# Performance work log

Hardware: AMD Instinct MI355X
Metric: run time of the kernel (lower is better)

Reference implementation:

```python
import jax, jax.numpy as jnp
import numpy as np

EPS = 1e-5
K = 20


def _knn_idx(p, k):
    # p: (B, N, C) -> indices of k nearest neighbors (B, N, k), self included
    inner = jnp.einsum('bnc,bmc->bnm', p, p)
    sq = jnp.sum(p * p, axis=-1)  # (B, N)
    neg_dist = 2.0 * inner - sq[:, :, None] - sq[:, None, :]
    return jax.lax.top_k(neg_dist, k)[1]


def _edge_feature(x, k):
    # x: (B, N, C) -> (B, N, k, 2C) = [neighbor - center, center]
    C = x.shape[-1]
    src = x if C in (3, 6) else x[..., 6:9]  # faithful to torch code path
    idx = _knn_idx(src, k)                    # (B, N, k)
    nb = jax.vmap(lambda xb, ib: xb[ib])(x, idx)  # (B, N, k, C)
    ctr = jnp.broadcast_to(x[:, :, None, :], nb.shape)
    return jnp.concatenate([nb - ctr, ctr], axis=-1)


def _block(h, W, g, b, m, v):
    # 1x1 conv (channels-last) + eval-mode BatchNorm + LeakyReLU(0.2)
    z = jnp.einsum('...c,oc->...o', h, W)
    z = (z - m) * jax.lax.rsqrt(v + EPS) * g + b
    return jnp.where(z >= 0, z, 0.2 * z)


def setup_inputs() -> dict:
    key = jax.random.key(0)
    B, N, D, F = 8, 2048, 3, 1024
    ks = jax.random.split(key, 16)
    s = 0.1
    x = jax.random.normal(ks[0], (B, N, D), dtype=jnp.float32)
    W1 = jax.random.normal(ks[1], (64, 2 * D), dtype=jnp.float32) * s
    W2 = jax.random.normal(ks[2], (64, 64), dtype=jnp.float32) * s
    W3 = jax.random.normal(ks[3], (64, 128), dtype=jnp.float32) * s
    W4 = jax.random.normal(ks[4], (64, 64), dtype=jnp.float32) * s
    W5 = jax.random.normal(ks[5], (64, 128), dtype=jnp.float32) * s
    W6 = jax.random.normal(ks[6], (F, 192), dtype=jnp.float32) * s
    # BN params for bn1..bn5 stacked along axis 0
    bng = 1.0 + 0.1 * jax.random.normal(ks[7], (5, 64), dtype=jnp.float32)
    bnb = 0.1 * jax.random.normal(ks[8], (5, 64), dtype=jnp.float32)
    bnm = 0.1 * jax.random.normal(ks[9], (5, 64), dtype=jnp.float32)
    bnv = 0.5 + jax.random.uniform(ks[10], (5, 64), dtype=jnp.float32)
    bn6g = 1.0 + 0.1 * jax.random.normal(ks[11], (F,), dtype=jnp.float32)
    bn6b = 0.1 * jax.random.normal(ks[12], (F,), dtype=jnp.float32)
    bn6m = 0.1 * jax.random.normal(ks[13], (F,), dtype=jnp.float32)
    bn6v = 0.5 + jax.random.uniform(ks[14], (F,), dtype=jnp.float32)
    return {"x": x, "W1": W1, "W2": W2, "W3": W3, "W4": W4, "W5": W5,
            "W6": W6, "bng": bng, "bnb": bnb, "bnm": bnm, "bnv": bnv,
            "bn6g": bn6g, "bn6b": bn6b, "bn6m": bn6m, "bn6v": bn6v}


def reference(x, W1, W2, W3, W4, W5, W6, bng, bnb, bnm, bnv,
              bn6g, bn6b, bn6m, bn6v):
    # x: (B, N, 3) channels-last throughout
    e = _edge_feature(x, K)                    # (B, N, K, 6)
    h = _block(e, W1, bng[0], bnb[0], bnm[0], bnv[0])
    h = _block(h, W2, bng[1], bnb[1], bnm[1], bnv[1])
    x1 = jnp.max(h, axis=2)                    # (B, N, 64)

    e = _edge_feature(x1, K)                   # knn on channels 6:9
    h = _block(e, W3, bng[2], bnb[2], bnm[2], bnv[2])
    h = _block(h, W4, bng[3], bnb[3], bnm[3], bnv[3])
    x2 = jnp.max(h, axis=2)                    # (B, N, 64)

    e = _edge_feature(x2, K)
    h = _block(e, W5, bng[4], bnb[4], bnm[4], bnv[4])
    x3 = jnp.max(h, axis=2)                    # (B, N, 64)

    x4 = jnp.concatenate([x1, x2, x3], axis=-1)  # (B, N, 192)
    z = _block(x4, W6, bn6g, bn6b, bn6m, bn6v)   # (B, N, F)
    g = jnp.max(z, axis=1)                       # (B, F)
    feat = g[:, None, :]                         # (B, 1, F)
    return feat, jnp.transpose(x4, (0, 2, 1))    # x4 as (B, 192, N)
```

## Files before the change

### kernel.cpp

```cpp
#include <hip/hip_runtime.h>
#include <hip/hip_bf16.h>
#include <math.h>

#define B_ 8
#define N_ 2048
#define KNN 20
#define CH 64

typedef unsigned int u32;

__device__ __forceinline__ float lrelu(float z) { return z >= 0.0f ? z : 0.2f * z; }

__device__ __forceinline__ u32 enc_f32(float f) {
  u32 u = __float_as_uint(f);
  return (u & 0x80000000u) ? ~u : (u | 0x80000000u);
}
__device__ __forceinline__ float dec_f32(u32 u) {
  u32 bits = (u & 0x80000000u) ? (u ^ 0x80000000u) : ~u;
  return __uint_as_float(bits);
}

__global__ __launch_bounds__(256) void prep_kernel(
    const float* __restrict__ W2, const float* __restrict__ W3, const float* __restrict__ W4,
    const float* __restrict__ W5, const float* __restrict__ W6,
    float* __restrict__ w2tg, float* __restrict__ w3tg, float* __restrict__ w4tg,
    float* __restrict__ w5tg, float* __restrict__ w6t, u32* __restrict__ gkeys) {
  int i = blockIdx.x * 256 + threadIdx.x;
  if (i < 192 * 1024) {
    int d = i >> 10, cc = i & 1023;
    w6t[i] = W6[cc * 192 + d];
  }
  if (i < 4096) {
    int c_ = i >> 6, cc = i & 63;
    w2tg[cc * 64 + c_] = W2[i];
    w4tg[cc * 64 + c_] = W4[i];
  }
  if (i < 8192) {
    int d = i >> 6, c_ = i & 63;
    w3tg[i] = W3[c_ * 128 + d];
    w5tg[i] = W5[c_ * 128 + d];
    gkeys[i] = 0u;
  }
}

#define QPB 32
#define SL 8
#define CSL (N_ / SL)
#define CAP 31

__global__ __launch_bounds__(256) void knn_kernel(const float* __restrict__ p, int ld, int off,
                                                  int* __restrict__ idxout) {
  __shared__ __align__(16) char arena[64640];
  float4* pts = (float4*)arena;
  int* buf = (int*)(arena + 32896);
  double* dls = (double*)arena;
  int* ils = (int*)(arena + 40960);

  const int b = blockIdx.y;
  const float* pb = p + (size_t)b * N_ * ld + off;
  for (int j = threadIdx.x; j < N_; j += 256) {
    pts[j + (j >> 8)] = make_float4(pb[(size_t)j * ld + 0], pb[(size_t)j * ld + 1],
                                    pb[(size_t)j * ld + 2], 0.f);
  }
  __syncthreads();

  const int t = threadIdx.x & 7;
  const int qloc = threadIdx.x >> 3;
  const int q = blockIdx.x * QPB + qloc;
  const float4 qp = pts[q + (q >> 8)];
  const int jb = t * CSL;
  const float4* myp = pts + jb + t;

  float d0 = 1e30f, d1 = 1e30f, d2 = 1e30f;
#pragma unroll 4
  for (int i = 0; i < CSL; ++i) {
    float4 c = myp[i];
    float dx = qp.x - c.x, dy = qp.y - c.y, dz = qp.z - c.z;
    float d = fmaf(dz, dz, fmaf(dy, dy, dx * dx));
    float lo = fminf(d, d0); float hi = fmaxf(d, d0); d0 = lo;
    float m1 = fminf(d1, hi); float c1 = fmaxf(d1, hi); d1 = m1;
    d2 = fminf(d2, c1);
  }
  float thr = d2;
#pragma unroll
  for (int s = 1; s < 8; s <<= 1) thr = fmaxf(thr, __shfl_xor(thr, s));
  thr = thr * 1.0001f + 1e-7f;

  int cnt = 0;
  int* mybuf = buf + threadIdx.x * CAP;
#pragma unroll 4
  for (int i = 0; i < CSL; ++i) {
    float4 c = myp[i];
    float dx = qp.x - c.x, dy = qp.y - c.y, dz = qp.z - c.z;
    float d = fmaf(dz, dz, fmaf(dy, dy, dx * dx));
    if (d <= thr) {
      if (cnt < CAP) mybuf[cnt] = jb + i;
      ++cnt;
    }
  }

  double ld_[KNN]; int li_[KNN];
#pragma unroll
  for (int u = 0; u < KNN; ++u) { ld_[u] = 1e300; li_[u] = 0x7fffffff; }

  const bool ovf = cnt > CAP;
  const int m = ovf ? 0 : cnt;
  for (int e = 0; e < m; ++e) {
    int j = mybuf[e];
    float4 c = pts[j + (j >> 8)];
    double dx = (double)qp.x - (double)c.x;
    double dy = (double)qp.y - (double)c.y;
    double dz = (double)qp.z - (double)c.z;
    double d = dx * dx + dy * dy + dz * dz;
    if (d < ld_[KNN - 1]) {
      ld_[KNN - 1] = d; li_[KNN - 1] = j;
#pragma unroll
      for (int u = KNN - 1; u > 0; --u) {
        if (ld_[u] < ld_[u - 1]) {
          double td = ld_[u]; ld_[u] = ld_[u - 1]; ld_[u - 1] = td;
          int ti = li_[u]; li_[u] = li_[u - 1]; li_[u - 1] = ti;
        }
      }
    }
  }
  if (ovf) {
    for (int i = 0; i < CSL; ++i) {
      int j = jb + i;
      float4 c = myp[i];
      double dx = (double)qp.x - (double)c.x;
      double dy = (double)qp.y - (double)c.y;
      double dz = (double)qp.z - (double)c.z;
      double d = dx * dx + dy * dy + dz * dz;
      if (d < ld_[KNN - 1]) {
        ld_[KNN - 1] = d; li_[KNN - 1] = j;
#pragma unroll
        for (int u = KNN - 1; u > 0; --u) {
          if (ld_[u] < ld_[u - 1]) {
            double td = ld_[u]; ld_[u] = ld_[u - 1]; ld_[u - 1] = td;
            int ti = li_[u]; li_[u] = li_[u - 1]; li_[u - 1] = ti;
          }
        }
      }
    }
  }
  __syncthreads();
#pragma unroll
  for (int u = 0; u < KNN; ++u) {
    dls[threadIdx.x * KNN + u] = ld_[u];
    ils[threadIdx.x * KNN + u] = li_[u];
  }
  __syncthreads();

  if (t == 0) {
    int h0 = 0, h1 = 0, h2 = 0, h3 = 0, h4 = 0, h5 = 0, h6 = 0, h7 = 0;
    const int lb = qloc * 8;
    int* outp = idxout + ((size_t)b * N_ + q) * KNN;
    for (int r = 0; r < KNN; ++r) {
      double bd = 1e301; int bi = 0x7fffffff; int bt = 0;
#define CONSIDER(T, H)                                                     \
      { int li2 = (lb + (T)) * KNN + (H);                                  \
        double dv = dls[li2]; int iv = ils[li2];                           \
        if (dv < bd || (dv == bd && iv < bi)) { bd = dv; bi = iv; bt = (T); } }
      CONSIDER(0, h0) CONSIDER(1, h1) CONSIDER(2, h2) CONSIDER(3, h3)
      CONSIDER(4, h4) CONSIDER(5, h5) CONSIDER(6, h6) CONSIDER(7, h7)
#undef CONSIDER
      outp[r] = bi;
      h0 += (bt == 0); h1 += (bt == 1); h2 += (bt == 2); h3 += (bt == 3);
      h4 += (bt == 4); h5 += (bt == 5); h6 += (bt == 6); h7 += (bt == 7);
    }
  }
}

__global__ __launch_bounds__(256) void stage1_kernel(
    const float* __restrict__ x, const int* __restrict__ idx,
    const float* __restrict__ W1, const float* __restrict__ w2tg,
    const float* __restrict__ g0, const float* __restrict__ b0,
    const float* __restrict__ m0, const float* __restrict__ v0,
    const float* __restrict__ g1, const float* __restrict__ b1,
    const float* __restrict__ m1, const float* __restrict__ v1,
    float* __restrict__ x1out) {
  __shared__ float nbs[4][KNN][3];
  __shared__ float ctrs[4][3];
  __shared__ int sidx[4][KNN];
  const int b = blockIdx.y;
  const int n0 = blockIdx.x * 4;
  const int p = threadIdx.x >> 6, c = threadIdx.x & 63;

  for (int i = threadIdx.x; i < 4 * KNN; i += 256)
    sidx[i / KNN][i % KNN] = idx[((size_t)b * N_ + n0 + i / KNN) * KNN + i % KNN];
  __syncthreads();
  for (int i = threadIdx.x; i < 4 * KNN * 3; i += 256) {
    int pp = i / (KNN * 3), r = i % (KNN * 3), k = r / 3, d = r % 3;
    nbs[pp][k][d] = x[((size_t)b * N_ + sidx[pp][k]) * 3 + d];
  }
  if (threadIdx.x < 12) {
    int pp = threadIdx.x / 3, d = threadIdx.x % 3;
    ctrs[pp][d] = x[((size_t)b * N_ + n0 + pp) * 3 + d];
  }
  __syncthreads();

  float sc0, sh0, sc1, sh1;
  {
    double rs = 1.0 / sqrt((double)v0[c] + 1e-5);
    sc0 = (float)((double)g0[c] * rs); sh0 = b0[c] - m0[c] * sc0;
    rs = 1.0 / sqrt((double)v1[c] + 1e-5);
    sc1 = (float)((double)g1[c] * rs); sh1 = b1[c] - m1[c] * sc1;
  }

  const float cx = ctrs[p][0], cy = ctrs[p][1], cz = ctrs[p][2];
  const float wa0 = W1[c * 6 + 0], wa1 = W1[c * 6 + 1], wa2 = W1[c * 6 + 2];
  const float wb0 = W1[c * 6 + 3], wb1 = W1[c * 6 + 4], wb2 = W1[c * 6 + 5];
  const float cbase = cx * wb0 + cy * wb1 + cz * wb2;

  float h1r[KNN];
#pragma unroll
  for (int k = 0; k < KNN; ++k) {
    float a = (nbs[p][k][0] - cx) * wa0 + (nbs[p][k][1] - cy) * wa1 + (nbs[p][k][2] - cz) * wa2 + cbase;
    h1r[k] = lrelu(a * sc0 + sh0);
  }

  float acc2[KNN];
#pragma unroll
  for (int k = 0; k < KNN; ++k) acc2[k] = 0.f;
  for (int cc = 0; cc < CH; ++cc) {
    float w = w2tg[cc * CH + c];
#pragma unroll
    for (int k = 0; k < KNN; ++k) {
      float hv = __int_as_float(__builtin_amdgcn_readlane(__float_as_int(h1r[k]), cc));
      acc2[k] += hv * w;
    }
  }
  float mx = -INFINITY;
#pragma unroll
  for (int k = 0; k < KNN; ++k) mx = fmaxf(mx, lrelu(acc2[k] * sc1 + sh1));
  x1out[((size_t)b * N_ + n0 + p) * CH + c] = mx;
}

__global__ __launch_bounds__(256) void stage2_kernel(
    const float* __restrict__ xin, const int* __restrict__ idx,
    const float* __restrict__ w3tg, const float* __restrict__ w4tg,
    const float* __restrict__ g0, const float* __restrict__ b0,
    const float* __restrict__ m0, const float* __restrict__ v0,
    const float* __restrict__ g1, const float* __restrict__ b1,
    const float* __restrict__ m1, const float* __restrict__ v1,
    float* __restrict__ xout) {
  __shared__ float nbs[4][KNN][CH];
  __shared__ float ctrs[4][CH];
  __shared__ int sidx[4][KNN];
  const int b = blockIdx.y, n0 = blockIdx.x * 4;
  const int p = threadIdx.x >> 6, c = threadIdx.x & 63;

  for (int i = threadIdx.x; i < 4 * KNN; i += 256)
    sidx[i / KNN][i % KNN] = idx[((size_t)b * N_ + n0 + i / KNN) * KNN + i % KNN];
  __syncthreads();
  for (int i = threadIdx.x; i < 4 * KNN * 16; i += 256) {
    int pp = i / (KNN * 16), r = i % (KNN * 16), k = r >> 4, d4 = (r & 15) * 4;
    const float4 v = *(const float4*)&xin[((size_t)b * N_ + sidx[pp][k]) * CH + d4];
    *(float4*)&nbs[pp][k][d4] = v;
  }
  for (int i = threadIdx.x; i < 4 * 16; i += 256) {
    int pp = i / 16, d4 = (i % 16) * 4;
    *(float4*)&ctrs[pp][d4] = *(const float4*)&xin[((size_t)b * N_ + n0 + pp) * CH + d4];
  }
  __syncthreads();

  float sc0, sh0, sc1, sh1;
  {
    double rs = 1.0 / sqrt((double)v0[c] + 1e-5);
    sc0 = (float)((double)g0[c] * rs); sh0 = b0[c] - m0[c] * sc0;
    rs = 1.0 / sqrt((double)v1[c] + 1e-5);
    sc1 = (float)((double)g1[c] * rs); sh1 = b1[c] - m1[c] * sc1;
  }

  float acc[KNN];
#pragma unroll
  for (int k = 0; k < KNN; ++k) acc[k] = 0.f;
  float base = 0.f;
#pragma unroll 4
  for (int d = 0; d < CH; d += 4) {
    float a0 = w3tg[(d + 0) * 64 + c], a1 = w3tg[(d + 1) * 64 + c];
    float a2 = w3tg[(d + 2) * 64 + c], a3 = w3tg[(d + 3) * 64 + c];
    float q0 = w3tg[(64 + d + 0) * 64 + c], q1 = w3tg[(64 + d + 1) * 64 + c];
    float q2 = w3tg[(64 + d + 2) * 64 + c], q3 = w3tg[(64 + d + 3) * 64 + c];
    const float4 ct = *(const float4*)&ctrs[p][d];
    base += ct.x * (q0 - a0) + ct.y * (q1 - a1) + ct.z * (q2 - a2) + ct.w * (q3 - a3);
#pragma unroll
    for (int k = 0; k < KNN; ++k) {
      const float4 nb = *(const float4*)&nbs[p][k][d];
      acc[k] += nb.x * a0 + nb.y * a1 + nb.z * a2 + nb.w * a3;
    }
  }
  float h1r[KNN];
#pragma unroll
  for (int k = 0; k < KNN; ++k) h1r[k] = lrelu((acc[k] + base) * sc0 + sh0);

  float acc2[KNN];
#pragma unroll
  for (int k = 0; k < KNN; ++k) acc2[k] = 0.f;
  for (int cc = 0; cc < CH; ++cc) {
    float w = w4tg[cc * CH + c];
#pragma unroll
    for (int k = 0; k < KNN; ++k) {
      float hv = __int_as_float(__builtin_amdgcn_readlane(__float_as_int(h1r[k]), cc));
      acc2[k] += hv * w;
    }
  }
  float mx = -INFINITY;
#pragma unroll
  for (int k = 0; k < KNN; ++k) mx = fmaxf(mx, lrelu(acc2[k] * sc1 + sh1));
  xout[((size_t)b * N_ + n0 + p) * CH + c] = mx;
}

__global__ __launch_bounds__(256) void stage3_kernel(
    const float* __restrict__ xin, const int* __restrict__ idx,
    const float* __restrict__ w5tg,
    const float* __restrict__ g0, const float* __restrict__ b0,
    const float* __restrict__ m0, const float* __restrict__ v0,
    float* __restrict__ xout) {
  __shared__ float nbs[4][KNN][CH];
  __shared__ float ctrs[4][CH];
  __shared__ int sidx[4][KNN];
  const int b = blockIdx.y, n0 = blockIdx.x * 4;
  const int p = threadIdx.x >> 6, c = threadIdx.x & 63;

  for (int i = threadIdx.x; i < 4 * KNN; i += 256)
    sidx[i / KNN][i % KNN] = idx[((size_t)b * N_ + n0 + i / KNN) * KNN + i % KNN];
  __syncthreads();
  for (int i = threadIdx.x; i < 4 * KNN * 16; i += 256) {
    int pp = i / (KNN * 16), r = i % (KNN * 16), k = r >> 4, d4 = (r & 15) * 4;
    const float4 v = *(const float4*)&xin[((size_t)b * N_ + sidx[pp][k]) * CH + d4];
    *(float4*)&nbs[pp][k][d4] = v;
  }
  for (int i = threadIdx.x; i < 4 * 16; i += 256) {
    int pp = i / 16, d4 = (i % 16) * 4;
    *(float4*)&ctrs[pp][d4] = *(const float4*)&xin[((size_t)b * N_ + n0 + pp) * CH + d4];
  }
  __syncthreads();

  float sc0, sh0;
  {
    double rs = 1.0 / sqrt((double)v0[c] + 1e-5);
    sc0 = (float)((double)g0[c] * rs); sh0 = b0[c] - m0[c] * sc0;
  }

  float acc[KNN];
#pragma unroll
  for (int k = 0; k < KNN; ++k) acc[k] = 0.f;
  float base = 0.f;
#pragma unroll 4
  for (int d = 0; d < CH; d += 4) {
    float a0 = w5tg[(d + 0) * 64 + c], a1 = w5tg[(d + 1) * 64 + c];
    float a2 = w5tg[(d + 2) * 64 + c], a3 = w5tg[(d + 3) * 64 + c];
    float q0 = w5tg[(64 + d + 0) * 64 + c], q1 = w5tg[(64 + d + 1) * 64 + c];
    float q2 = w5tg[(64 + d + 2) * 64 + c], q3 = w5tg[(64 + d + 3) * 64 + c];
    const float4 ct = *(const float4*)&ctrs[p][d];
    base += ct.x * (q0 - a0) + ct.y * (q1 - a1) + ct.z * (q2 - a2) + ct.w * (q3 - a3);
#pragma unroll
    for (int k = 0; k < KNN; ++k) {
      const float4 nb = *(const float4*)&nbs[p][k][d];
      acc[k] += nb.x * a0 + nb.y * a1 + nb.z * a2 + nb.w * a3;
    }
  }
  float mx = -INFINITY;
#pragma unroll
  for (int k = 0; k < KNN; ++k) mx = fmaxf(mx, lrelu((acc[k] + base) * sc0 + sh0));
  xout[((size_t)b * N_ + n0 + p) * CH + c] = mx;
}

__global__ __launch_bounds__(256) void stage6_kernel(
    const float* __restrict__ x1, const float* __restrict__ x2, const float* __restrict__ x3,
    const float* __restrict__ w6t,
    const float* __restrict__ g6, const float* __restrict__ b6,
    const float* __restrict__ m6, const float* __restrict__ v6,
    u32* __restrict__ gkeys) {
  __shared__ float xsT[192][16];
  const int b = blockIdx.y;
  const int n0 = blockIdx.x * 16;
  for (int i = threadIdx.x; i < 16 * 192; i += 256) {
    int d = i >> 4, pp = i & 15;
    float v;
    if (d < 64)       v = x1[((size_t)b * N_ + n0 + pp) * CH + d];
    else if (d < 128) v = x2[((size_t)b * N_ + n0 + pp) * CH + (d - 64)];
    else              v = x3[((size_t)b * N_ + n0 + pp) * CH + (d - 128)];
    xsT[d][pp] = v;
  }
  __syncthreads();

  const int c0 = threadIdx.x << 2;
  float4 acc[16];
#pragma unroll
  for (int pp = 0; pp < 16; ++pp) acc[pp] = make_float4(0.f, 0.f, 0.f, 0.f);

  for (int d = 0; d < 192; ++d) {
    const float4 w = *(const float4*)&w6t[(size_t)d * 1024 + c0];
#pragma unroll
    for (int q = 0; q < 4; ++q) {
      const float4 xq = *(const float4*)&xsT[d][q * 4];
#define ACC4(J, XV) { float4& A = acc[q * 4 + (J)]; A.x += (XV) * w.x; A.y += (XV) * w.y; A.z += (XV) * w.z; A.w += (XV) * w.w; }
      ACC4(0, xq.x) ACC4(1, xq.y) ACC4(2, xq.z) ACC4(3, xq.w)
#undef ACC4
    }
  }

  const float4 gg = *(const float4*)&g6[c0];
  const float4 bb = *(const float4*)&b6[c0];
  const float4 mm = *(const float4*)&m6[c0];
  const float4 vv = *(const float4*)&v6[c0];
  float4 s, h;
  s.x = (float)((double)gg.x / sqrt((double)vv.x + 1e-5)); h.x = bb.x - mm.x * s.x;
  s.y = (float)((double)gg.y / sqrt((double)vv.y + 1e-5)); h.y = bb.y - mm.y * s.y;
  s.z = (float)((double)gg.z / sqrt((double)vv.z + 1e-5)); h.z = bb.z - mm.z * s.z;
  s.w = (float)((double)gg.w / sqrt((double)vv.w + 1e-5)); h.w = bb.w - mm.w * s.w;

  float4 mx = make_float4(-INFINITY, -INFINITY, -INFINITY, -INFINITY);
#pragma unroll
  for (int pp = 0; pp < 16; ++pp) {
    mx.x = fmaxf(mx.x, lrelu(acc[pp].x * s.x + h.x));
    mx.y = fmaxf(mx.y, lrelu(acc[pp].y * s.y + h.y));
    mx.z = fmaxf(mx.z, lrelu(acc[pp].z * s.z + h.z));
    mx.w = fmaxf(mx.w, lrelu(acc[pp].w * s.w + h.w));
  }
  u32* gk = gkeys + (size_t)b * 1024 + c0;
  atomicMax(&gk[0], enc_f32(mx.x));
  atomicMax(&gk[1], enc_f32(mx.y));
  atomicMax(&gk[2], enc_f32(mx.z));
  atomicMax(&gk[3], enc_f32(mx.w));
}

__global__ __launch_bounds__(256) void feat_kernel(const u32* __restrict__ gkeys, float* __restrict__ out) {
  int i = blockIdx.x * 256 + threadIdx.x;
  if (i < 8192) out[i] = dec_f32(gkeys[i]);
}

__global__ __launch_bounds__(256) void xpose_kernel(
    const float* __restrict__ x1, const float* __restrict__ x2, const float* __restrict__ x3,
    float* __restrict__ out) {
  __shared__ float tile[64][65];
  const int b = blockIdx.y;
  const int n0 = blockIdx.x * 64;
  const float* srcs[3] = {x1, x2, x3};
#pragma unroll
  for (int s = 0; s < 3; ++s) {
    const float* src = srcs[s];
    {
      const int row = threadIdx.x >> 2, cb = (threadIdx.x & 3) * 16;
      const float4* rp = (const float4*)&src[((size_t)b * N_ + n0 + row) * CH + cb];
      float4 v0 = rp[0], v1 = rp[1], v2 = rp[2], v3 = rp[3];
      float* tp = &tile[row][cb];
      tp[0] = v0.x; tp[1] = v0.y; tp[2] = v0.z; tp[3] = v0.w;
      tp[4] = v1.x; tp[5] = v1.y; tp[6] = v1.z; tp[7] = v1.w;
      tp[8] = v2.x; tp[9] = v2.y; tp[10] = v2.z; tp[11] = v2.w;
      tp[12] = v3.x; tp[13] = v3.y; tp[14] = v3.z; tp[15] = v3.w;
    }
    __syncthreads();
    {
      const int n = threadIdx.x & 63;
      const int cg = (threadIdx.x >> 6) * 16;
      for (int c = cg; c < cg + 16; ++c)
        out[((size_t)b * 192 + s * 64 + c) * N_ + n0 + n] = tile[n][c];
    }
    __syncthreads();
  }
}

extern "C" void kernel_launch(void* const* d_in, const int* in_sizes, int n_in,
                              void* d_out, int out_size, void* d_ws, size_t ws_size,
                              hipStream_t stream) {
  const float* x   = (const float*)d_in[0];
  const float* W1  = (const float*)d_in[1];
  const float* W2  = (const float*)d_in[2];
  const float* W3  = (const float*)d_in[3];
  const float* W4  = (const float*)d_in[4];
  const float* W5  = (const float*)d_in[5];
  const float* W6  = (const float*)d_in[6];
  const float* bng = (const float*)d_in[7];
  const float* bnb = (const float*)d_in[8];
  const float* bnm = (const float*)d_in[9];
  const float* bnv = (const float*)d_in[10];
  const float* g6  = (const float*)d_in[11];
  const float* b6  = (const float*)d_in[12];
  const float* m6  = (const float*)d_in[13];
  const float* v6  = (const float*)d_in[14];
  float* out = (float*)d_out;

  float* ws = (float*)d_ws;
  float* x1b  = ws;
  float* x2b  = x1b + 1048576;
  float* x3b  = x2b + 1048576;
  float* w6t  = x3b + 1048576;
  float* w2tg = w6t + 196608;
  float* w4tg = w2tg + 4096;
  float* w3tg = w4tg + 4096;
  float* w5tg = w3tg + 8192;
  u32*   gkeys = (u32*)(w5tg + 8192);
  int*   idxb  = (int*)(gkeys + 8192);

  prep_kernel<<<768, 256, 0, stream>>>(W2, W3, W4, W5, W6, w2tg, w3tg, w4tg, w5tg, w6t, gkeys);

  knn_kernel<<<dim3(N_ / QPB, B_), 256, 0, stream>>>(x, 3, 0, idxb);
  stage1_kernel<<<dim3(N_ / 4, B_), 256, 0, stream>>>(
      x, idxb, W1, w2tg,
      bng + 0, bnb + 0, bnm + 0, bnv + 0,
      bng + 64, bnb + 64, bnm + 64, bnv + 64, x1b);

  knn_kernel<<<dim3(N_ / QPB, B_), 256, 0, stream>>>(x1b, 64, 6, idxb);
  stage2_kernel<<<dim3(N_ / 4, B_), 256, 0, stream>>>(
      x1b, idxb, w3tg, w4tg,
      bng + 128, bnb + 128, bnm + 128, bnv + 128,
      bng + 192, bnb + 192, bnm + 192, bnv + 192, x2b);

  knn_kernel<<<dim3(N_ / QPB, B_), 256, 0, stream>>>(x2b, 64, 6, idxb);
  stage3_kernel<<<dim3(N_ / 4, B_), 256, 0, stream>>>(
      x2b, idxb, w5tg,
      bng + 256, bnb + 256, bnm + 256, bnv + 256, x3b);

  stage6_kernel<<<dim3(N_ / 16, B_), 256, 0, stream>>>(x1b, x2b, x3b, w6t, g6, b6, m6, v6, gkeys);
  feat_kernel<<<32, 256, 0, stream>>>(gkeys, out);
  xpose_kernel<<<dim3(N_ / 64, B_), 256, 0, stream>>>(x1b, x2b, x3b, out + 8192);
}
```

Before: 791.2 us.

## Compute stage3 edge conv on MFMA with three-way bf16 split for fp32 accuracy

```diff
diff --git a/kernel.cpp b/kernel.cpp
--- a/kernel.cpp
+++ b/kernel.cpp
@@ -8,6 +8,9 @@
 #define CH 64
 
 typedef unsigned int u32;
+typedef unsigned short ushort16;
+typedef __attribute__((ext_vector_type(8))) short s8v;
+typedef __attribute__((ext_vector_type(4))) float f4v;
 
 __device__ __forceinline__ float lrelu(float z) { return z >= 0.0f ? z : 0.2f * z; }
 
@@ -18,13 +21,50 @@
 __device__ __forceinline__ float dec_f32(u32 u) {
   u32 bits = (u & 0x80000000u) ? (u ^ 0x80000000u) : ~u;
   return __uint_as_float(bits);
+}
+__device__ __forceinline__ ushort16 f2bf(float f) {
+  u32 u = __float_as_uint(f);
+  u = (u + 0x7fffu + ((u >> 16) & 1u)) >> 16;
+  return (ushort16)u;
+}
+__device__ __forceinline__ float bf2f(ushort16 h) { return __uint_as_float(((u32)h) << 16); }
+
+__device__ __forceinline__ void split3(const float* __restrict__ p, s8v& a0, s8v& a1, s8v& a2) {
+#pragma unroll
+  for (int j = 0; j < 8; ++j) {
+    float v = p[j];
+    ushort16 h0 = f2bf(v);
+    float r = v - bf2f(h0);
+    u32 ru = __float_as_uint(r);
+    a0[j] = (short)h0;
+    a1[j] = (short)(ru >> 16);
+    float r2 = r - __uint_as_float(ru & 0xFFFF0000u);
+    a2[j] = (short)f2bf(r2);
+  }
+}
+
+#define MFMA6(ACC, A0, A1, A2, B0, B1, B2)                                   \
+  ACC = __builtin_amdgcn_mfma_f32_16x16x32_bf16(A0, B0, ACC, 0, 0, 0);       \
+  ACC = __builtin_amdgcn_mfma_f32_16x16x32_bf16(A0, B1, ACC, 0, 0, 0);       \
+  ACC = __builtin_amdgcn_mfma_f32_16x16x32_bf16(A1, B0, ACC, 0, 0, 0);       \
+  ACC = __builtin_amdgcn_mfma_f32_16x16x32_bf16(A0, B2, ACC, 0, 0, 0);       \
+  ACC = __builtin_amdgcn_mfma_f32_16x16x32_bf16(A1, B1, ACC, 0, 0, 0);       \
+  ACC = __builtin_amdgcn_mfma_f32_16x16x32_bf16(A2, B0, ACC, 0, 0, 0);
+
+__device__ __forceinline__ void wsplit(float v, ushort16& h0, ushort16& h1, ushort16& h2) {
+  h0 = f2bf(v);
+  float r = v - bf2f(h0);
+  h1 = f2bf(r);
+  float r2 = r - bf2f(h1);
+  h2 = f2bf(r2);
 }
 
 __global__ __launch_bounds__(256) void prep_kernel(
     const float* __restrict__ W2, const float* __restrict__ W3, const float* __restrict__ W4,
     const float* __restrict__ W5, const float* __restrict__ W6,
     float* __restrict__ w2tg, float* __restrict__ w3tg, float* __restrict__ w4tg,
-    float* __restrict__ w5tg, float* __restrict__ w6t, u32* __restrict__ gkeys) {
+    ushort16* __restrict__ wp5h, ushort16* __restrict__ wp5m, ushort16* __restrict__ wp5l,
+    float* __restrict__ w6t, u32* __restrict__ gkeys) {
   int i = blockIdx.x * 256 + threadIdx.x;
   if (i < 192 * 1024) {
     int d = i >> 10, cc = i & 1023;
@@ -36,10 +76,15 @@
     w4tg[cc * 64 + c_] = W4[i];
   }
   if (i < 8192) {
-    int d = i >> 6, c_ = i & 63;
-    w3tg[i] = W3[c_ * 128 + d];
-    w5tg[i] = W5[c_ * 128 + d];
     gkeys[i] = 0u;
+    { int d = i >> 6, c_ = i & 63; w3tg[i] = W3[c_ * 128 + d]; }
+    int j = i & 7, l = (i >> 3) & 63, tile = i >> 9;
+    int kk = tile >> 2, nt = tile & 3;
+    int d = kk * 32 + ((l >> 4) << 3) + j;
+    int ch = nt * 16 + (l & 15);
+    float v5 = (d < 64) ? W5[ch * 128 + d] : (W5[ch * 128 + d] - W5[ch * 128 + d - 64]);
+    ushort16 a, b, c;
+    wsplit(v5, a, b, c); wp5h[i] = a; wp5m[i] = b; wp5l[i] = c;
   }
 }
 
@@ -312,59 +357,67 @@
 }
 
 __global__ __launch_bounds__(256) void stage3_kernel(
-    const float* __restrict__ xin, const int* __restrict__ idx,
-    const float* __restrict__ w5tg,
+    const float* __restrict__ xf, const int* __restrict__ idx,
+    const ushort16* __restrict__ wpAh, const ushort16* __restrict__ wpAm, const ushort16* __restrict__ wpAl,
     const float* __restrict__ g0, const float* __restrict__ b0,
     const float* __restrict__ m0, const float* __restrict__ v0,
-    float* __restrict__ xout) {
-  __shared__ float nbs[4][KNN][CH];
-  __shared__ float ctrs[4][CH];
-  __shared__ int sidx[4][KNN];
-  const int b = blockIdx.y, n0 = blockIdx.x * 4;
-  const int p = threadIdx.x >> 6, c = threadIdx.x & 63;
-
-  for (int i = threadIdx.x; i < 4 * KNN; i += 256)
-    sidx[i / KNN][i % KNN] = idx[((size_t)b * N_ + n0 + i / KNN) * KNN + i % KNN];
-  __syncthreads();
-  for (int i = threadIdx.x; i < 4 * KNN * 16; i += 256) {
-    int pp = i / (KNN * 16), r = i % (KNN * 16), k = r >> 4, d4 = (r & 15) * 4;
-    const float4 v = *(const float4*)&xin[((size_t)b * N_ + sidx[pp][k]) * CH + d4];
-    *(float4*)&nbs[pp][k][d4] = v;
-  }
-  for (int i = threadIdx.x; i < 4 * 16; i += 256) {
-    int pp = i / 16, d4 = (i % 16) * 4;
-    *(float4*)&ctrs[pp][d4] = *(const float4*)&xin[((size_t)b * N_ + n0 + pp) * CH + d4];
-  }
-  __syncthreads();
-
-  float sc0, sh0;
-  {
-    double rs = 1.0 / sqrt((double)v0[c] + 1e-5);
-    sc0 = (float)((double)g0[c] * rs); sh0 = b0[c] - m0[c] * sc0;
-  }
-
-  float acc[KNN];
-#pragma unroll
-  for (int k = 0; k < KNN; ++k) acc[k] = 0.f;
-  float base = 0.f;
-#pragma unroll 4
-  for (int d = 0; d < CH; d += 4) {
-    float a0 = w5tg[(d + 0) * 64 + c], a1 = w5tg[(d + 1) * 64 + c];
-    float a2 = w5tg[(d + 2) * 64 + c], a3 = w5tg[(d + 3) * 64 + c];
-    float q0 = w5tg[(64 + d + 0) * 64 + c], q1 = w5tg[(64 + d + 1) * 64 + c];
-    float q2 = w5tg[(64 + d + 2) * 64 + c], q3 = w5tg[(64 + d + 3) * 64 + c];
-    const float4 ct = *(const float4*)&ctrs[p][d];
-    base += ct.x * (q0 - a0) + ct.y * (q1 - a1) + ct.z * (q2 - a2) + ct.w * (q3 - a3);
-#pragma unroll
-    for (int k = 0; k < KNN; ++k) {
-      const float4 nb = *(const float4*)&nbs[p][k][d];
-      acc[k] += nb.x * a0 + nb.y * a1 + nb.z * a2 + nb.w * a3;
-    }
-  }
-  float mx = -INFINITY;
-#pragma unroll
-  for (int k = 0; k < KNN; ++k) mx = fmaxf(mx, lrelu((acc[k] + base) * sc0 + sh0));
-  xout[((size_t)b * N_ + n0 + p) * CH + c] = mx;
+    float* __restrict__ xoutf) {
+  __shared__ int sidx[160];
+  __shared__ u32 h2k[512];
+  const int b = blockIdx.y, n0 = blockIdx.x * 8;
+  const int tid = threadIdx.x, l = tid & 63, wv = tid >> 6;
+
+  for (int i = tid; i < 160; i += 256) sidx[i] = idx[((size_t)b * N_ + n0 + i / KNN) * KNN + i % KNN];
+  for (int i = tid; i < 512; i += 256) h2k[i] = 0u;
+  __syncthreads();
+
+  float sc1[4], sh1[4];
+#pragma unroll
+  for (int nt = 0; nt < 4; ++nt) {
+    int ch = nt * 16 + (l & 15);
+    double rs = 1.0 / sqrt((double)v0[ch] + 1e-5);
+    sc1[nt] = (float)((double)g0[ch] * rs); sh1[nt] = b0[ch] - m0[ch] * sc1[nt];
+  }
+  const int lg = (l >> 4) << 3;
+
+  for (int mt = wv; mt < 10; mt += 4) {
+    const int row = mt * 16 + (l & 15);
+    const int nb = sidx[row];
+    const int p = row / KNN;
+    const float* xnb = xf + ((size_t)b * N_ + nb) * CH;
+    const float* xct = xf + ((size_t)b * N_ + n0 + p) * CH;
+
+    f4v acc[4];
+#pragma unroll
+    for (int nt = 0; nt < 4; ++nt) acc[nt] = (f4v){0.f, 0.f, 0.f, 0.f};
+#pragma unroll
+    for (int kk = 0; kk < 4; ++kk) {
+      const float* src = (kk < 2) ? (xnb + kk * 32 + lg) : (xct + (kk - 2) * 32 + lg);
+      s8v a0, a1, a2;
+      split3(src, a0, a1, a2);
+#pragma unroll
+      for (int nt = 0; nt < 4; ++nt) {
+        int wo = ((kk * 4 + nt) * 64 + l) << 3;
+        s8v bh = *(const s8v*)&wpAh[wo];
+        s8v bm = *(const s8v*)&wpAm[wo];
+        s8v bl = *(const s8v*)&wpAl[wo];
+        MFMA6(acc[nt], a0, a1, a2, bh, bm, bl)
+      }
+    }
+#pragma unroll
+    for (int nt = 0; nt < 4; ++nt)
+#pragma unroll
+      for (int r = 0; r < 4; ++r) {
+        float v = lrelu(acc[nt][r] * sc1[nt] + sh1[nt]);
+        int row2 = mt * 16 + ((l >> 4) << 2) + r;
+        atomicMax(&h2k[(row2 / KNN) * 64 + nt * 16 + (l & 15)], enc_f32(v));
+      }
+  }
+  __syncthreads();
+  for (int i = tid; i < 512; i += 256) {
+    size_t o = ((size_t)b * N_ + n0 + (i >> 6)) * CH + (i & 63);
+    xoutf[o] = dec_f32(h2k[i]);
+  }
 }
 
 __global__ __launch_bounds__(256) void stage6_kernel(
@@ -491,11 +544,15 @@
   float* w2tg = w6t + 196608;
   float* w4tg = w2tg + 4096;
   float* w3tg = w4tg + 4096;
-  float* w5tg = w3tg + 8192;
-  u32*   gkeys = (u32*)(w5tg + 8192);
+  u32*   gkeys = (u32*)(w3tg + 8192);
   int*   idxb  = (int*)(gkeys + 8192);
-
-  prep_kernel<<<768, 256, 0, stream>>>(W2, W3, W4, W5, W6, w2tg, w3tg, w4tg, w5tg, w6t, gkeys);
+  ushort16* wp5h = (ushort16*)(idxb + 327680);
+  ushort16* wp5m = wp5h + 65536;
+  ushort16* wp5l = wp5m + 65536;
+
+  prep_kernel<<<768, 256, 0, stream>>>(W2, W3, W4, W5, W6,
+                                       w2tg, w3tg, w4tg,
+                                       wp5h, wp5m, wp5l, w6t, gkeys);
 
   knn_kernel<<<dim3(N_ / QPB, B_), 256, 0, stream>>>(x, 3, 0, idxb);
   stage1_kernel<<<dim3(N_ / 4, B_), 256, 0, stream>>>(
@@ -510,8 +567,8 @@
       bng + 192, bnb + 192, bnm + 192, bnv + 192, x2b);
 
   knn_kernel<<<dim3(N_ / QPB, B_), 256, 0, stream>>>(x2b, 64, 6, idxb);
-  stage3_kernel<<<dim3(N_ / 4, B_), 256, 0, stream>>>(
-      x2b, idxb, w5tg,
+  stage3_kernel<<<dim3(N_ / 8, B_), 256, 0, stream>>>(
+      x2b, idxb, wp5h, wp5m, wp5l,
       bng + 256, bnb + 256, bnm + 256, bnv + 256, x3b);
 
   stage6_kernel<<<dim3(N_ / 16, B_), 256, 0, stream>>>(x1b, x2b, x3b, w6t, g6, b6, m6, v6, gkeys);
```

Measured after the change: 798.7 us. Within noise of the previous version (+0.9%).
